# Kernel optimization log

Measured on AMD Instinct MI355X. Metric: run time of the kernel, lower is better.

## Reference

```python
import jax, jax.numpy as jnp
import numpy as np
from jax import lax

N = 4096        # number of nodes (= number of hyperedges)
F_DIM = 256     # feature_dim
E_DIM = 128     # embed_dim
K = 9           # hardcoded k_neig in forward


def setup_inputs() -> dict:
    key = jax.random.key(0)
    ks = jax.random.split(key, 10)
    x = jax.random.normal(ks[0], (N, F_DIM), jnp.float32)
    # distance/similarity matrix; continuous values avoid argsort tie ambiguity
    XY_Adj = jax.random.uniform(ks[1], (N, N), jnp.float32)

    def unif(k, shape, fan_out):  # torch HGNN_conv init: U(-1/sqrt(out), 1/sqrt(out))
        s = 1.0 / np.sqrt(fan_out)
        return jax.random.uniform(k, shape, jnp.float32, -s, s)

    W10 = unif(ks[2], (F_DIM, E_DIM), E_DIM); b10 = unif(ks[3], (E_DIM,), E_DIM)
    W11 = unif(ks[4], (E_DIM, E_DIM), E_DIM); b11 = unif(ks[5], (E_DIM,), E_DIM)
    W20 = unif(ks[6], (E_DIM, E_DIM), E_DIM); b20 = unif(ks[7], (E_DIM,), E_DIM)
    W21 = unif(ks[8], (E_DIM, F_DIM), F_DIM); b21 = unif(ks[9], (F_DIM,), F_DIM)
    return {"x": x, "XY_Adj": XY_Adj,
            "W10": W10, "b10": b10, "W11": W11, "b11": b11,
            "W20": W20, "b20": b20, "W21": W21, "b21": b21}


def _build_G(dis, k):
    """Vectorized construct_H_with_KNN_from_distance + _generate_G_from_H.
    Picks the k LARGEST entries per row (original does reversed argsort),
    forces the center node into its own hyperedge, builds binary H [N,N]
    (rows=nodes, cols=hyperedges), then G = DV^-1/2 H DE^-1 H^T DV^-1/2 (W=I)."""
    n = dis.shape[0]
    centers = jnp.arange(n)
    dis = jnp.where(jnp.eye(n, dtype=bool), 0.0, dis)  # zero the diagonal
    _, idx = lax.top_k(dis, k)                         # [N, k] descending per row
    has_center = (idx == centers[:, None]).any(axis=1)
    idx = idx.at[:, k - 1].set(jnp.where(has_center, idx[:, k - 1], centers))
    H = jnp.zeros((n, n), dis.dtype).at[idx, centers[:, None]].set(1.0)
    DV = H.sum(axis=1)                                 # node degrees (>=1)
    DE = H.sum(axis=0)                                 # hyperedge degrees (=k)
    dv2 = DV ** -0.5
    left = dv2[:, None] * H * (1.0 / DE)[None, :]      # DV^-1/2 H DE^-1
    G = left @ (H.T * dv2[None, :])                    # ... H^T DV^-1/2
    return G


def _hgnn(x, G, W1, b1, W2, b2):
    # HGNN: relu(G(xW1+b1)) -> dropout (identity in eval) -> G(hW2+b2)
    h = jax.nn.relu(G @ (x @ W1 + b1))
    return G @ (h @ W2 + b2)


def reference(x, XY_Adj, W10, b10, W11, b11, W20, b20, W21, b21):
    G = _build_G(XY_Adj, K)
    x1 = jax.nn.relu(_hgnn(x, G, W10, b10, W11, b11))
    x2 = jax.nn.relu(_hgnn(x1, G, W20, b20, W21, b21))
    return (x, x1, x2)
```

## Files before the change

kernel.cpp:

```cpp
#include <hip/hip_runtime.h>

#define N_NODES 4096
#define KNN 9
#define CAPS 128
#define CAPE 32
#define THRESH 0.99f
#define GEMMB 1024

__device__ __forceinline__ bool vi_greater(float av, int aj, float bv, int bj) {
  return (av > bv) || (av == bv && aj < bj);
}

__global__ __launch_bounds__(256) void s0_kernel(const float* __restrict__ x,
                                                 const float* __restrict__ adj,
                                                 const float* __restrict__ W10,
                                                 const float* __restrict__ b10,
                                                 float* __restrict__ P,
                                                 float* __restrict__ xcopy,
                                                 int* __restrict__ cur,
                                                 int* __restrict__ idx) {
  __shared__ float sf[1024];
  __shared__ int   si[512];
  const int tid = threadIdx.x;

  if (blockIdx.x < GEMMB) {
    int gid = blockIdx.x * 256 + tid;
    if (gid < N_NODES) cur[gid] = 0;
    int m0 = blockIdx.x * 4;
    {
      float4 y4 = reinterpret_cast<const float4*>(x + (size_t)m0 * 256)[tid];
      reinterpret_cast<float4*>(sf)[tid] = y4;
      reinterpret_cast<float4*>(xcopy + (size_t)m0 * 256)[tid] = y4;
    }
    __syncthreads();
    const int f  = tid & 127;
    const int rb = (tid >> 7) * 2;
    float a0 = 0.f, a1 = 0.f;
    for (int k = 0; k < 256; k += 4) {
      float w0 = W10[(k + 0) * 128 + f];
      float w1 = W10[(k + 1) * 128 + f];
      float w2 = W10[(k + 2) * 128 + f];
      float w3 = W10[(k + 3) * 128 + f];
      float4 y0 = *reinterpret_cast<const float4*>(&sf[(rb + 0) * 256 + k]);
      float4 y1 = *reinterpret_cast<const float4*>(&sf[(rb + 1) * 256 + k]);
      a0 = fmaf(y0.x, w0, fmaf(y0.y, w1, fmaf(y0.z, w2, fmaf(y0.w, w3, a0))));
      a1 = fmaf(y1.x, w0, fmaf(y1.y, w1, fmaf(y1.z, w2, fmaf(y1.w, w3, a1))));
    }
    float bb = b10[f];
    P[(size_t)(m0 + rb + 0) * 128 + f] = a0 + bb;
    P[(size_t)(m0 + rb + 1) * 128 + f] = a1 + bb;
  } else {
    const int lane = tid & 63, wv = tid >> 6;
    const int row = (blockIdx.x - GEMMB) * 4 + wv;
    const float4* r4 = reinterpret_cast<const float4*>(adj + (size_t)row * N_NODES);
    float* wval = sf + wv * CAPS;
    int*   widx = si + wv * CAPS;
    const unsigned long long lmask = (1ull << lane) - 1;

    int n = 0;
#pragma unroll 4
    for (int t = 0; t < 16; ++t) {
      float4 f4 = r4[t * 64 + lane];
      float vals[4] = {f4.x, f4.y, f4.z, f4.w};
      int cb = (t * 64 + lane) * 4;
#pragma unroll
      for (int q = 0; q < 4; ++q) {
        int cc = cb + q;
        bool pred = (vals[q] > THRESH) && (cc != row);
        unsigned long long m = __ballot(pred);
        if (pred) {
          int p = n + __popcll(m & lmask);
          if (p < CAPS) { wval[p] = vals[q]; widx[p] = cc; }
        }
        n += __popcll(m);
      }
    }
    __syncthreads();

    int outj[KNN];
    if (n >= 8 && n <= CAPS) {
      float v0 = -3.0e38f, v1 = -3.0e38f;
      int c0 = 0x7fffffff, c1 = 0x7fffffff;
      if (lane < n)      { v0 = wval[lane];      c0 = widx[lane]; }
      if (lane + 64 < n) { v1 = wval[lane + 64]; c1 = widx[lane + 64]; }
#pragma unroll
      for (int rnd = 0; rnd < 8; ++rnd) {
        bool first = vi_greater(v0, c0, v1, c1);
        float mv = first ? v0 : v1;
        int   mc = first ? c0 : c1;
#pragma unroll
        for (int d = 1; d < 64; d <<= 1) {
          float ov = __shfl_xor(mv, d);
          int   oc = __shfl_xor(mc, d);
          if (vi_greater(ov, oc, mv, mc)) { mv = ov; mc = oc; }
        }
        outj[rnd] = mc;
        if (c0 == mc) v0 = -3.3e38f;
        if (c1 == mc) v1 = -3.3e38f;
      }
      outj[8] = row;
    } else {
      const float* r = adj + (size_t)row * N_NODES;
      float v[9]; int ji[9];
#pragma unroll
      for (int t = 0; t < 9; ++t) { v[t] = -3.0e38f; ji[t] = 0x7fffffff; }
      for (int t = 0; t < 64; ++t) {
        int cc = t * 64 + lane;
        float val = (cc == row) ? 0.0f : r[cc];
        if (vi_greater(val, cc, v[8], ji[8])) {
          v[8] = val; ji[8] = cc;
#pragma unroll
          for (int s = 8; s > 0; --s) {
            if (vi_greater(v[s], ji[s], v[s-1], ji[s-1])) {
              float tv = v[s]; v[s] = v[s-1]; v[s-1] = tv;
              int tj = ji[s]; ji[s] = ji[s-1]; ji[s-1] = tj;
            }
          }
        }
      }
      bool has_center = false;
#pragma unroll
      for (int rnd = 0; rnd < 9; ++rnd) {
        float mv = v[0]; int mj = ji[0];
#pragma unroll
        for (int d = 1; d < 64; d <<= 1) {
          float ov = __shfl_xor(mv, d);
          int   oj = __shfl_xor(mj, d);
          if (vi_greater(ov, oj, mv, mj)) { mv = ov; mj = oj; }
        }
        outj[rnd] = mj;
        has_center = has_center || (mj == row);
        if (ji[0] == mj) {
#pragma unroll
          for (int s = 0; s < 8; ++s) { v[s] = v[s+1]; ji[s] = ji[s+1]; }
          v[8] = -3.0e38f; ji[8] = 0x7fffffff;
        }
      }
      if (!has_center) outj[8] = row;
    }
    if (lane < KNN) idx[row * KNN + lane] = outj[lane];
  }
}

__global__ void build_elist(const int* __restrict__ idx, int* __restrict__ cur,
                            int* __restrict__ elist) {
  int t = blockIdx.x * blockDim.x + threadIdx.x;
  if (t >= N_NODES * KNN) return;
  int node = idx[t];
  int p = atomicAdd(&cur[node], 1);
  if (p < CAPE) elist[node * CAPE + p] = t / KNN;
}

template<int F>
__global__ __launch_bounds__(F) void edge_gather(const float* __restrict__ Y,
                                                 const int* __restrict__ idx,
                                                 const int* __restrict__ DV,
                                                 float* __restrict__ Z) {
  __shared__ int er[KNN];
  __shared__ float ew[KNN];
  int e = blockIdx.x;
  if (threadIdx.x < KNN) {
    int r = idx[e * KNN + threadIdx.x];
    er[threadIdx.x] = r;
    ew[threadIdx.x] = rsqrtf((float)DV[r]);
  }
  __syncthreads();
  int f = threadIdx.x;
  float acc = 0.f;
#pragma unroll
  for (int j = 0; j < KNN; ++j)
    acc = fmaf(ew[j], Y[(size_t)er[j] * F + f], acc);
  Z[(size_t)e * F + f] = acc * (1.0f / 9.0f);
}

template<int KD>
__device__ __forceinline__ float node_acc(const float* __restrict__ Z,
                                          const int* __restrict__ elist,
                                          int i, int f, int cnt) {
  const int4* el4 = reinterpret_cast<const int4*>(elist + i * CAPE);
  int4 ea = el4[0], eb = el4[1], ec = el4[2], ed = el4[3];
  int e1[16] = {ea.x, ea.y, ea.z, ea.w, eb.x, eb.y, eb.z, eb.w,
                ec.x, ec.y, ec.z, ec.w, ed.x, ed.y, ed.z, ed.w};
  float acc = 0.f;
#pragma unroll
  for (int j = 0; j < 16; ++j) {
    float m = (j < cnt) ? 1.0f : 0.0f;
    acc = fmaf(m, Z[(size_t)(e1[j] & (N_NODES - 1)) * KD + f], acc);
  }
  for (int t = 16; t < cnt; ++t)
    acc += Z[(size_t)elist[i * CAPE + t] * KD + f];
  return acc;
}

template<int F>
__global__ __launch_bounds__(F) void node_gather(const float* __restrict__ Z,
                                                 const int* __restrict__ elist,
                                                 const int* __restrict__ DV,
                                                 float* __restrict__ out) {
  int i = blockIdx.x;
  int f = threadIdx.x;
  int cnt = DV[i]; if (cnt > CAPE) cnt = CAPE;
  float acc = node_acc<F>(Z, elist, i, f, cnt);
  out[(size_t)i * F + f] = fmaxf(acc * rsqrtf((float)DV[i]), 0.f);
}

template<int FO, bool WRITE_H>
__global__ __launch_bounds__(256) void node_gemm(const float* __restrict__ Z,
                                                 const int* __restrict__ elist,
                                                 const int* __restrict__ DV,
                                                 const float* __restrict__ W,
                                                 const float* __restrict__ bias,
                                                 float* __restrict__ P,
                                                 float* __restrict__ Hout) {
  constexpr int KD = 128;
  constexpr int ROWS = 8;
  constexpr int RPT = (FO == 128) ? 4 : 8;
  __shared__ float ylds[ROWS * KD];
  int m0 = blockIdx.x * ROWS;
#pragma unroll
  for (int c0 = 0; c0 < ROWS * KD; c0 += 256) {
    int cell = c0 + threadIdx.x;
    int rr = cell >> 7, f = cell & 127;
    int i = m0 + rr;
    int cnt = DV[i]; if (cnt > CAPE) cnt = CAPE;
    float acc = node_acc<KD>(Z, elist, i, f, cnt);
    acc = fmaxf(acc * rsqrtf((float)DV[i]), 0.f);
    ylds[cell] = acc;
    if (WRITE_H) Hout[(size_t)i * KD + f] = acc;
  }
  __syncthreads();
  const int f  = (FO == 128) ? (threadIdx.x & 127) : threadIdx.x;
  const int rb = (FO == 128) ? ((threadIdx.x >> 7) * 4) : 0;
  float acc[RPT];
#pragma unroll
  for (int rr = 0; rr < RPT; ++rr) acc[rr] = 0.f;
  for (int k = 0; k < KD; k += 4) {
    float w0 = W[(size_t)(k + 0) * FO + f];
    float w1 = W[(size_t)(k + 1) * FO + f];
    float w2 = W[(size_t)(k + 2) * FO + f];
    float w3 = W[(size_t)(k + 3) * FO + f];
#pragma unroll
    for (int rr = 0; rr < RPT; ++rr) {
      float4 y = *reinterpret_cast<const float4*>(&ylds[(rb + rr) * KD + k]);
      acc[rr] = fmaf(y.x, w0, fmaf(y.y, w1, fmaf(y.z, w2, fmaf(y.w, w3, acc[rr]))));
    }
  }
  float bb = bias[f];
#pragma unroll
  for (int rr = 0; rr < RPT; ++rr)
    P[(size_t)(m0 + rb + rr) * FO + f] = acc[rr] + bb;
}

extern "C" void kernel_launch(void* const* d_in, const int* in_sizes, int n_in,
                              void* d_out, int out_size, void* d_ws, size_t ws_size,
                              hipStream_t stream) {
  const float* x   = (const float*)d_in[0];
  const float* adj = (const float*)d_in[1];
  const float* W10 = (const float*)d_in[2];
  const float* b10 = (const float*)d_in[3];
  const float* W11 = (const float*)d_in[4];
  const float* b11 = (const float*)d_in[5];
  const float* W20 = (const float*)d_in[6];
  const float* b20 = (const float*)d_in[7];
  const float* W21 = (const float*)d_in[8];
  const float* b21 = (const float*)d_in[9];
  float* out = (float*)d_out;

  char* w = (char*)d_ws;
  int*   idx   = (int*)(w + 0);
  int*   cur   = (int*)(w + 147456);
  int*   elist = (int*)(w + 163840);
  float* bufP  = (float*)(w + 688128);
  float* bufZ  = (float*)(w + 4882432);

  float* x1out = out + (size_t)N_NODES * 256;
  float* x2out = x1out + (size_t)N_NODES * 128;

  s0_kernel<<<2 * GEMMB, 256, 0, stream>>>(x, adj, W10, b10, bufP, out, cur, idx);
  build_elist<<<(N_NODES * KNN + 255) / 256, 256, 0, stream>>>(idx, cur, elist);

  edge_gather<128><<<N_NODES, 128, 0, stream>>>(bufP, idx, cur, bufZ);
  node_gemm<128, false><<<N_NODES / 8, 256, 0, stream>>>(bufZ, elist, cur,
                                                         W11, b11, bufP, nullptr);
  edge_gather<128><<<N_NODES, 128, 0, stream>>>(bufP, idx, cur, bufZ);
  node_gemm<128, true><<<N_NODES / 8, 256, 0, stream>>>(bufZ, elist, cur,
                                                        W20, b20, bufP, x1out);
  edge_gather<128><<<N_NODES, 128, 0, stream>>>(bufP, idx, cur, bufZ);
  node_gemm<256, false><<<N_NODES / 8, 256, 0, stream>>>(bufZ, elist, cur,
                                                         W21, b21, bufP, nullptr);
  edge_gather<256><<<N_NODES, 256, 0, stream>>>(bufP, idx, cur, bufZ);
  node_gather<256><<<N_NODES, 256, 0, stream>>>(bufZ, elist, cur, x2out);
}
```

Before: 98.37 us.

## Replace serial shuffle argmax top-8 with rank-counting selection and reorder blocks

The KNN selection branch now ranks each thresholded candidate by counting how many candidates beat it in shared memory, and writes it straight to its slot. This replaces the eight rounds of 64-lane shuffle reductions. The kNN rows are moved to the low block indices so they are scheduled before the GEMM blocks, the diagonal check moves out of the scan loop, and the fallback path writes its output through scalars instead of a dynamically indexed array. The cost is an O(n) serial loop over shared memory per lane, and the __syncthreads is dropped, which relies on each wave only reading its own shared-memory slice.

```diff
diff --git a/kernel.cpp b/kernel.cpp
--- a/kernel.cpp
+++ b/kernel.cpp
@@ -24,9 +24,111 @@
   const int tid = threadIdx.x;
 
   if (blockIdx.x < GEMMB) {
-    int gid = blockIdx.x * 256 + tid;
+    const int lane = tid & 63, wv = tid >> 6;
+    const int row = blockIdx.x * 4 + wv;
+    const float4* r4 = reinterpret_cast<const float4*>(adj + (size_t)row * N_NODES);
+    float* wval = sf + wv * CAPS;
+    int*   widx = si + wv * CAPS;
+    const unsigned long long lmask = (1ull << lane) - 1;
+
+    int n = 0;
+#pragma unroll 4
+    for (int t = 0; t < 16; ++t) {
+      float4 f4 = r4[t * 64 + lane];
+      float vals[4] = {f4.x, f4.y, f4.z, f4.w};
+      int cb = (t * 64 + lane) * 4;
+#pragma unroll
+      for (int q = 0; q < 4; ++q) {
+        bool pred = (vals[q] > THRESH);
+        unsigned long long m = __ballot(pred);
+        if (pred) {
+          int p = n + __popcll(m & lmask);
+          if (p < CAPS) { wval[p] = vals[q]; widx[p] = cb + q; }
+        }
+        n += __popcll(m);
+      }
+    }
+
+    if (n >= 9 && n <= CAPS) {
+      bool val0 = lane < n, val1 = lane + 64 < n;
+      float v0 = 0.f, v1 = 0.f; int c0 = -1, c1 = -1;
+      if (val0) { v0 = wval[lane];      c0 = widx[lane]; }
+      if (val1) { v1 = wval[lane + 64]; c1 = widx[lane + 64]; }
+      if (c0 == row) val0 = false;
+      if (c1 == row) val1 = false;
+      int r0 = 0, r1 = 0;
+      if (n <= 64) {
+        for (int s = 0; s < n; ++s) {
+          float vs = wval[s]; int cs = widx[s];
+          if (cs != row && vi_greater(vs, cs, v0, c0)) ++r0;
+        }
+      } else {
+        for (int s = 0; s < n; ++s) {
+          float vs = wval[s]; int cs = widx[s];
+          bool d = (cs != row);
+          if (d && vi_greater(vs, cs, v0, c0)) ++r0;
+          if (d && vi_greater(vs, cs, v1, c1)) ++r1;
+        }
+      }
+      if (val0 && r0 < 8) idx[row * KNN + r0] = c0;
+      if (val1 && r1 < 8) idx[row * KNN + r1] = c1;
+      if (lane == 0)      idx[row * KNN + 8] = row;
+    } else {
+      const float* r = adj + (size_t)row * N_NODES;
+      float v[9]; int ji[9];
+#pragma unroll
+      for (int t = 0; t < 9; ++t) { v[t] = -3.0e38f; ji[t] = 0x7fffffff; }
+      for (int t = 0; t < 64; ++t) {
+        int cc = t * 64 + lane;
+        float val = (cc == row) ? 0.0f : r[cc];
+        if (vi_greater(val, cc, v[8], ji[8])) {
+          v[8] = val; ji[8] = cc;
+#pragma unroll
+          for (int s = 8; s > 0; --s) {
+            if (vi_greater(v[s], ji[s], v[s-1], ji[s-1])) {
+              float tv = v[s]; v[s] = v[s-1]; v[s-1] = tv;
+              int tj = ji[s]; ji[s] = ji[s-1]; ji[s-1] = tj;
+            }
+          }
+        }
+      }
+      int o0=0,o1=0,o2=0,o3=0,o4=0,o5=0,o6=0,o7=0,o8=0;
+      bool has_center = false;
+#pragma unroll
+      for (int rnd = 0; rnd < 9; ++rnd) {
+        float mv = v[0]; int mj = ji[0];
+#pragma unroll
+        for (int d = 1; d < 64; d <<= 1) {
+          float ov = __shfl_xor(mv, d);
+          int   oj = __shfl_xor(mj, d);
+          if (vi_greater(ov, oj, mv, mj)) { mv = ov; mj = oj; }
+        }
+        switch (rnd) {
+          case 0: o0 = mj; break; case 1: o1 = mj; break;
+          case 2: o2 = mj; break; case 3: o3 = mj; break;
+          case 4: o4 = mj; break; case 5: o5 = mj; break;
+          case 6: o6 = mj; break; case 7: o7 = mj; break;
+          default: o8 = mj; break;
+        }
+        has_center = has_center || (mj == row);
+        if (ji[0] == mj) {
+#pragma unroll
+          for (int s = 0; s < 8; ++s) { v[s] = v[s+1]; ji[s] = ji[s+1]; }
+          v[8] = -3.0e38f; ji[8] = 0x7fffffff;
+        }
+      }
+      if (!has_center) o8 = row;
+      if (lane == 0) {
+        int* ip = idx + row * KNN;
+        ip[0]=o0; ip[1]=o1; ip[2]=o2; ip[3]=o3; ip[4]=o4;
+        ip[5]=o5; ip[6]=o6; ip[7]=o7; ip[8]=o8;
+      }
+    }
+  } else {
+    int bb0 = blockIdx.x - GEMMB;
+    int gid = bb0 * 256 + tid;
     if (gid < N_NODES) cur[gid] = 0;
-    int m0 = blockIdx.x * 4;
+    int m0 = bb0 * 4;
     {
       float4 y4 = reinterpret_cast<const float4*>(x + (size_t)m0 * 256)[tid];
       reinterpret_cast<float4*>(sf)[tid] = y4;
@@ -49,96 +151,6 @@
     float bb = b10[f];
     P[(size_t)(m0 + rb + 0) * 128 + f] = a0 + bb;
     P[(size_t)(m0 + rb + 1) * 128 + f] = a1 + bb;
-  } else {
-    const int lane = tid & 63, wv = tid >> 6;
-    const int row = (blockIdx.x - GEMMB) * 4 + wv;
-    const float4* r4 = reinterpret_cast<const float4*>(adj + (size_t)row * N_NODES);
-    float* wval = sf + wv * CAPS;
-    int*   widx = si + wv * CAPS;
-    const unsigned long long lmask = (1ull << lane) - 1;
-
-    int n = 0;
-#pragma unroll 4
-    for (int t = 0; t < 16; ++t) {
-      float4 f4 = r4[t * 64 + lane];
-      float vals[4] = {f4.x, f4.y, f4.z, f4.w};
-      int cb = (t * 64 + lane) * 4;
-#pragma unroll
-      for (int q = 0; q < 4; ++q) {
-        int cc = cb + q;
-        bool pred = (vals[q] > THRESH) && (cc != row);
-        unsigned long long m = __ballot(pred);
-        if (pred) {
-          int p = n + __popcll(m & lmask);
-          if (p < CAPS) { wval[p] = vals[q]; widx[p] = cc; }
-        }
-        n += __popcll(m);
-      }
-    }
-    __syncthreads();
-
-    int outj[KNN];
-    if (n >= 8 && n <= CAPS) {
-      float v0 = -3.0e38f, v1 = -3.0e38f;
-      int c0 = 0x7fffffff, c1 = 0x7fffffff;
-      if (lane < n)      { v0 = wval[lane];      c0 = widx[lane]; }
-      if (lane + 64 < n) { v1 = wval[lane + 64]; c1 = widx[lane + 64]; }
-#pragma unroll
-      for (int rnd = 0; rnd < 8; ++rnd) {
-        bool first = vi_greater(v0, c0, v1, c1);
-        float mv = first ? v0 : v1;
-        int   mc = first ? c0 : c1;
-#pragma unroll
-        for (int d = 1; d < 64; d <<= 1) {
-          float ov = __shfl_xor(mv, d);
-          int   oc = __shfl_xor(mc, d);
-          if (vi_greater(ov, oc, mv, mc)) { mv = ov; mc = oc; }
-        }
-        outj[rnd] = mc;
-        if (c0 == mc) v0 = -3.3e38f;
-        if (c1 == mc) v1 = -3.3e38f;
-      }
-      outj[8] = row;
-    } else {
-      const float* r = adj + (size_t)row * N_NODES;
-      float v[9]; int ji[9];
-#pragma unroll
-      for (int t = 0; t < 9; ++t) { v[t] = -3.0e38f; ji[t] = 0x7fffffff; }
-      for (int t = 0; t < 64; ++t) {
-        int cc = t * 64 + lane;
-        float val = (cc == row) ? 0.0f : r[cc];
-        if (vi_greater(val, cc, v[8], ji[8])) {
-          v[8] = val; ji[8] = cc;
-#pragma unroll
-          for (int s = 8; s > 0; --s) {
-            if (vi_greater(v[s], ji[s], v[s-1], ji[s-1])) {
-              float tv = v[s]; v[s] = v[s-1]; v[s-1] = tv;
-              int tj = ji[s]; ji[s] = ji[s-1]; ji[s-1] = tj;
-            }
-          }
-        }
-      }
-      bool has_center = false;
-#pragma unroll
-      for (int rnd = 0; rnd < 9; ++rnd) {
-        float mv = v[0]; int mj = ji[0];
-#pragma unroll
-        for (int d = 1; d < 64; d <<= 1) {
-          float ov = __shfl_xor(mv, d);
-          int   oj = __shfl_xor(mj, d);
-          if (vi_greater(ov, oj, mv, mj)) { mv = ov; mj = oj; }
-        }
-        outj[rnd] = mj;
-        has_center = has_center || (mj == row);
-        if (ji[0] == mj) {
-#pragma unroll
-          for (int s = 0; s < 8; ++s) { v[s] = v[s+1]; ji[s] = ji[s+1]; }
-          v[8] = -3.0e38f; ji[8] = 0x7fffffff;
-        }
-      }
-      if (!has_center) outj[8] = row;
-    }
-    if (lane < KNN) idx[row * KNN + lane] = outj[lane];
   }
 }
 
```

New measurement: 93.67 us. -4.8%, faster.
